# Kernel tuning notes

Hardware: AMD Instinct MI355X
Metric: run time of the kernel (lower is better)

Reference implementation:

```python
import jax, jax.numpy as jnp
import numpy as np

D_MODEL = 1024
NUM_HEADS = 16


def setup_inputs() -> dict:
    key = jax.random.key(0)
    ks = jax.random.split(key, 5)
    B, N, D = 2, 2048, D_MODEL
    x = jax.random.normal(ks[0], (B, N, D), dtype=jnp.float32)
    Wq = jax.random.normal(ks[1], (D, D), dtype=jnp.float32) * 0.02
    Wk = jax.random.normal(ks[2], (D, D), dtype=jnp.float32) * 0.02
    Wv = jax.random.normal(ks[3], (D, D), dtype=jnp.float32) * 0.02
    Wo = jax.random.normal(ks[4], (D, D), dtype=jnp.float32) * 0.02
    return {"x": x, "Wq": Wq, "Wk": Wk, "Wv": Wv, "Wo": Wo}


def reference(x, Wq, Wk, Wv, Wo):
    # Executed path of QuantizedHyperbolicAttention.forward: TRITON_AVAILABLE is
    # False in the source, so the module always runs _pytorch_attention
    # (standard scaled-dot-product attention), mask=None.
    B, N, D = x.shape
    H = NUM_HEADS
    hd = D // H
    # nn.Linear(bias=False): y = x @ W.T
    q = (x @ Wq.T).reshape(B, N, H, hd).transpose(0, 2, 1, 3)  # [B,H,N,hd]
    k = (x @ Wk.T).reshape(B, N, H, hd).transpose(0, 2, 1, 3)
    v = (x @ Wv.T).reshape(B, N, H, hd).transpose(0, 2, 1, 3)
    scale = hd ** -0.5
    attn = jnp.einsum("bhnd,bhmd->bhnm", q, k) * scale  # [B,H,N,N]
    attn = jax.nn.softmax(attn, axis=-1)
    out = jnp.einsum("bhnm,bhmd->bhnd", attn, v)  # [B,H,N,hd]
    out = out.transpose(0, 2, 1, 3).reshape(B, N, D)
    return out @ Wo.T
```

## Files before the change

kernel.cpp:

```cpp
#include <hip/hip_runtime.h>

using u16 = unsigned short;
using u32 = unsigned int;

typedef __bf16 bf16x8 __attribute__((ext_vector_type(8)));
typedef float  f32x4  __attribute__((ext_vector_type(4)));
typedef float  f32x8  __attribute__((ext_vector_type(8)));
typedef float  f32x16 __attribute__((ext_vector_type(16)));
typedef u16    u16x8  __attribute__((ext_vector_type(8)));
typedef u32    u32x4  __attribute__((ext_vector_type(4)));

#if __has_builtin(__builtin_amdgcn_exp2f)
#define QSCALE 0.1803368801f
__device__ __forceinline__ float fexp(float x) { return __builtin_amdgcn_exp2f(x); }
#else
#define QSCALE 0.125f
__device__ __forceinline__ float fexp(float x) { return __expf(x); }
#endif

__device__ __forceinline__ u32 f2bf(float f) {
  u32 u = __builtin_bit_cast(u32, f);
  return (u + 0x7fffu + ((u >> 16) & 1u)) >> 16;
}

__device__ __forceinline__ void gload_lds16(const u16* g, u16* lds) {
  __builtin_amdgcn_global_load_lds(
      (const __attribute__((address_space(1))) void*)g,
      (__attribute__((address_space(3))) void*)lds, 16, 0, 0);
}

__device__ __forceinline__ u32 cvtpk(float lo, float hi) {
  u32 r;
  asm("v_cvt_pk_bf16_f32 %0, %1, %2" : "=v"(r) : "v"(lo), "v"(hi));
  return r;
}

__device__ __forceinline__ float xhalf_add(float v) {
  return v + __shfl_xor(v, 32);
}

__global__ __launch_bounds__(256) void cvt_all(
    const float* __restrict__ x,  const float* __restrict__ wq,
    const float* __restrict__ wk, const float* __restrict__ wv,
    const float* __restrict__ wo, u16* __restrict__ out) {
  size_t i = ((size_t)blockIdx.x * 256 + threadIdx.x) * 16;
  const float* src;
  if (i < 4194304) {
    src = x + i;
  } else {
    size_t j = i - 4194304;
    unsigned w = (unsigned)(j >> 20);
    size_t o = j & 1048575;
    src = (w == 0) ? (wq + o) : (w == 1) ? (wk + o) : (w == 2) ? (wv + o) : (wo + o);
  }
  f32x4 a = *(const f32x4*)src;
  f32x4 b = *(const f32x4*)(src + 4);
  f32x4 c = *(const f32x4*)(src + 8);
  f32x4 d = *(const f32x4*)(src + 12);
  u32x4 r0, r1;
  r0[0] = f2bf(a[0]) | (f2bf(a[1]) << 16);
  r0[1] = f2bf(a[2]) | (f2bf(a[3]) << 16);
  r0[2] = f2bf(b[0]) | (f2bf(b[1]) << 16);
  r0[3] = f2bf(b[2]) | (f2bf(b[3]) << 16);
  r1[0] = f2bf(c[0]) | (f2bf(c[1]) << 16);
  r1[1] = f2bf(c[2]) | (f2bf(c[3]) << 16);
  r1[2] = f2bf(d[0]) | (f2bf(d[1]) << 16);
  r1[3] = f2bf(d[2]) | (f2bf(d[3]) << 16);
  *(u32x4*)(out + i) = r0;
  *(u32x4*)(out + i + 8) = r1;
}

template <bool F32OUT, int BM>
__device__ __forceinline__ void gemm_tile(const u16* __restrict__ A,
                                          const u16* __restrict__ Bm,
                                          void* __restrict__ Cv,
                                          int rowBase, int colBase, float scale) {
  __shared__ __align__(16) u16 As[BM * 64];
  __shared__ __align__(16) u16 Bs[128 * 64];

  const int t = threadIdx.x;
  const int lane = t & 63;
  const int wv = t >> 6;
  const int wr = (wv >> 1) * (BM / 2);
  const int wc = (wv & 1) * 64;
  const int l15 = lane & 15;
  const int lg = lane >> 4;

  f32x4 acc[BM / 32][4] = {};

  for (int kt = 0; kt < 1024; kt += 64) {
#pragma unroll
    for (int i = 0; i < BM / 32; ++i) {
      int s = i * 256 + t;
      int row = s >> 3;
      int k2 = (s & 7) ^ (row & 7);
      gload_lds16(A + (size_t)(rowBase + row) * 1024 + kt + k2 * 8,
                  &As[(i * 256 + wv * 64) * 8]);
    }
#pragma unroll
    for (int i = 0; i < 4; ++i) {
      int s = i * 256 + t;
      int row = s >> 3;
      int k2 = (s & 7) ^ (row & 7);
      gload_lds16(Bm + (size_t)(colBase + row) * 1024 + kt + k2 * 8,
                  &Bs[(i * 256 + wv * 64) * 8]);
    }
    __syncthreads();
#pragma unroll
    for (int kk = 0; kk < 2; ++kk) {
      bf16x8 af[BM / 32], bfr[4];
#pragma unroll
      for (int m = 0; m < BM / 32; ++m) {
        int row = wr + m * 16 + l15;
        af[m] = *(const bf16x8*)&As[row * 64 + (((kk * 4 + lg) ^ (row & 7)) * 8)];
      }
#pragma unroll
      for (int n = 0; n < 4; ++n) {
        int row = wc + n * 16 + l15;
        bfr[n] = *(const bf16x8*)&Bs[row * 64 + (((kk * 4 + lg) ^ (row & 7)) * 8)];
      }
      __builtin_amdgcn_s_setprio(1);
#pragma unroll
      for (int m = 0; m < BM / 32; ++m)
#pragma unroll
        for (int n = 0; n < 4; ++n)
          acc[m][n] = __builtin_amdgcn_mfma_f32_16x16x32_bf16(af[m], bfr[n], acc[m][n], 0, 0, 0);
      __builtin_amdgcn_s_setprio(0);
    }
    __syncthreads();
  }

#pragma unroll
  for (int m = 0; m < BM / 32; ++m) {
#pragma unroll
    for (int r = 0; r < 4; ++r) {
      int row = rowBase + wr + m * 16 + lg * 4 + r;
#pragma unroll
      for (int n = 0; n < 4; ++n) {
        int col = colBase + wc + n * 16 + l15;
        float v = acc[m][n][r] * scale;
        if (F32OUT)
          ((float*)Cv)[(size_t)row * 1024 + col] = v;
        else
          ((u16*)Cv)[(size_t)row * 1024 + col] = (u16)f2bf(v);
      }
    }
  }
}

__global__ __launch_bounds__(256) void gemm_qkv(
    const u16* __restrict__ xb,
    const u16* __restrict__ wq, const u16* __restrict__ wk, const u16* __restrict__ wv,
    u16* __restrict__ Qm, u16* __restrict__ Km, u16* __restrict__ Vm) {
  int bx = blockIdx.x;
  int mat = bx >> 8;
  int rem = bx & 255;
  int bm = rem & 31, bn = rem >> 5;
  const u16* B = (mat == 0) ? wq : (mat == 1) ? wk : wv;
  u16* C = (mat == 0) ? Qm : (mat == 1) ? Km : Vm;
  float scale = (mat == 0) ? QSCALE : 1.0f;
  gemm_tile<false, 128>(xb, B, C, bm * 128, bn * 128, scale);
}

__global__ __launch_bounds__(256) void gemm_out(
    const u16* __restrict__ ao, const u16* __restrict__ wo, float* __restrict__ C) {
  int bm = blockIdx.x & 63, bn = blockIdx.x >> 6;
  gemm_tile<true, 64>(ao, wo, C, bm * 64, bn * 128, 1.0f);
}

__global__ __launch_bounds__(512, 2) void attn_fwd(
    const u16* __restrict__ Q, const u16* __restrict__ K,
    const u16* __restrict__ V, u16* __restrict__ AO) {
  __shared__ __align__(16) u16 Ks[2][2][64 * 64];
  __shared__ __align__(16) u16 Vt3[2][3][64 * 64];

  const int t = threadIdx.x;
  const int lane = t & 63;
  const int wvi = t >> 6;
  const int wg = wvi & 3;
  const int grp = wvi >> 2;
  const int tg = t & 255;
  const int l31 = lane & 31;
  const int hi = lane >> 5;

  const int qb = blockIdx.x;
  const int pr = blockIdx.y;
  const size_t hb = (size_t)(pr >> 4) * 2048 * 1024 + (size_t)(pr & 15) * 64;
  const u16* Qh = Q + hb;
  const u16* Kh = K + hb;
  const u16* Vh = V + hb;
  u16* AOh = AO + hb;

  const int q0w = qb * 128 + wg * 32;
  const int kvb = grp * 1024;

  bf16x8 qf[4];
#pragma unroll
  for (int kk = 0; kk < 4; ++kk)
    qf[kk] = *(const bf16x8*)&Qh[(size_t)(q0w + l31) * 1024 + kk * 16 + hi * 8];

  f32x16 ot[2] = {};
  f32x16 sc[2];
  f32x8  Lacc = {};
  bf16x8 pa0[4], pa1[4];

  const int kxor = l31 & 7;
  const int kd0 = (l31 & 7) ^ (l31 >> 3);
  const int kv0 = (tg >> 3) * 2, d0 = (tg & 7) * 8;
  const int vg = (kv0 >> 4) * 2 + ((kv0 >> 2) & 1);
  const int vj = (kv0 & 3) + ((kv0 >> 3) & 1) * 4;

  auto VLOAD = [&](int tile, u16x8& a, u16x8& b) {
    a = *(const u16x8*)&Vh[(size_t)(kvb + tile * 64 + kv0) * 1024 + d0];
    b = *(const u16x8*)&Vh[(size_t)(kvb + tile * 64 + kv0 + 1) * 1024 + d0];
  };
  auto KSTAGE = [&](int tile, int buf) {
#pragma unroll
    for (int i = 0; i < 2; ++i) {
      int s = i * 256 + tg;
      int krow = s >> 3;
      int k2 = (s & 7) ^ (krow & 7);
      gload_lds16(&Kh[(size_t)(kvb + tile * 64 + krow) * 1024 + k2 * 8],
                  &Ks[grp][buf][(i * 256 + wg * 64) * 8]);
    }
  };
  auto VPACK = [&](u16x8 a, u16x8 b, u16* dst) {
#pragma unroll
    for (int e = 0; e < 8; ++e) {
      int d = d0 + e;
      int key = ((d & 7) ^ (d >> 3)) & 7;
      int idx = d * 64 + ((vg ^ key) * 8) + vj;
      *(u32*)&dst[idx] = (u32)a[e] | ((u32)b[e] << 16);
    }
  };
  auto QKT = [&](const u16* ks) {
    sc[0] = f32x16{};
    sc[1] = f32x16{};
    __builtin_amdgcn_s_setprio(1);
#pragma unroll
    for (int kk = 0; kk < 4; ++kk) {
      bf16x8 kf0 = *(const bf16x8*)&ks[l31 * 64 + (((kk * 2 + hi) ^ kxor) * 8)];
      bf16x8 kf1 = *(const bf16x8*)&ks[(32 + l31) * 64 + (((kk * 2 + hi) ^ kxor) * 8)];
      sc[0] = __builtin_amdgcn_mfma_f32_32x32x16_bf16(kf0, qf[kk], sc[0], 0, 0, 0);
      sc[1] = __builtin_amdgcn_mfma_f32_32x32x16_bf16(kf1, qf[kk], sc[1], 0, 0, 0);
    }
    __builtin_amdgcn_s_setprio(0);
  };
  auto PV = [&](const u16* vt, const bf16x8* pa) {
    __builtin_amdgcn_s_setprio(1);
#pragma unroll
    for (int kk = 0; kk < 4; ++kk) {
      bf16x8 vf0 = *(const bf16x8*)&vt[l31 * 64 + (((kk * 2 + hi) ^ kd0) * 8)];
      bf16x8 vf1 = *(const bf16x8*)&vt[(32 + l31) * 64 + (((kk * 2 + hi) ^ (kd0 ^ 4)) * 8)];
      ot[0] = __builtin_amdgcn_mfma_f32_32x32x16_bf16(vf0, pa[kk], ot[0], 0, 0, 0);
      ot[1] = __builtin_amdgcn_mfma_f32_32x32x16_bf16(vf1, pa[kk], ot[1], 0, 0, 0);
    }
    __builtin_amdgcn_s_setprio(0);
  };
  auto EXPPACK = [&](bf16x8* pa) {
#pragma unroll
    for (int fi = 0; fi < 2; ++fi)
#pragma unroll
      for (int r = 0; r < 16; ++r)
        sc[fi][r] = fexp(sc[fi][r]);
    {
      f32x8 lo0 = __builtin_shufflevector(sc[0], sc[0], 0,1,2,3,4,5,6,7);
      f32x8 hi0 = __builtin_shufflevector(sc[0], sc[0], 8,9,10,11,12,13,14,15);
      f32x8 lo1 = __builtin_shufflevector(sc[1], sc[1], 0,1,2,3,4,5,6,7);
      f32x8 hi1 = __builtin_shufflevector(sc[1], sc[1], 8,9,10,11,12,13,14,15);
      Lacc += (lo0 + hi0) + (lo1 + hi1);
    }
#pragma unroll
    for (int fi = 0; fi < 2; ++fi) {
      u32x4 w0 = {cvtpk(sc[fi][0],  sc[fi][1]),  cvtpk(sc[fi][2],  sc[fi][3]),
                  cvtpk(sc[fi][4],  sc[fi][5]),  cvtpk(sc[fi][6],  sc[fi][7])};
      u32x4 w1 = {cvtpk(sc[fi][8],  sc[fi][9]),  cvtpk(sc[fi][10], sc[fi][11]),
                  cvtpk(sc[fi][12], sc[fi][13]), cvtpk(sc[fi][14], sc[fi][15])};
      pa[2 * fi]     = __builtin_bit_cast(bf16x8, w0);
      pa[2 * fi + 1] = __builtin_bit_cast(bf16x8, w1);
    }
  };

  int vm1 = 2, v0 = 0, vp1 = 1;
  auto ROT = [&]() { int tmp = vm1; vm1 = v0; v0 = vp1; vp1 = tmp; };

  {
    u16x8 a, b;
    VLOAD(0, a, b);
    __builtin_amdgcn_sched_barrier(0);
    KSTAGE(0, 0);
    KSTAGE(1, 1);
    VPACK(a, b, &Vt3[grp][0][0]);
    asm volatile("s_waitcnt vmcnt(2)" ::: "memory");
    asm volatile("s_waitcnt lgkmcnt(0)" ::: "memory");
    __builtin_amdgcn_sched_barrier(0);
    __builtin_amdgcn_s_barrier();
    QKT(&Ks[grp][0][0]);
    asm volatile("s_waitcnt lgkmcnt(0)" ::: "memory");
    __builtin_amdgcn_sched_barrier(0);
    __builtin_amdgcn_s_barrier();
  }

  for (int tp = 0; tp < 7; ++tp) {
#pragma unroll
    for (int sub = 0; sub < 2; ++sub) {
      const int tt = 2 * tp + sub;
      u16x8 a, b;
      VLOAD(tt + 1, a, b);
      __builtin_amdgcn_sched_barrier(0);
      KSTAGE(tt + 2, sub);
      if (tt >= 1) PV(&Vt3[grp][vm1][0], sub ? pa0 : pa1);
      EXPPACK(sub ? pa1 : pa0);
      asm volatile("s_waitcnt vmcnt(4)" ::: "memory");
      QKT(&Ks[grp][sub ^ 1][0]);
      VPACK(a, b, &Vt3[grp][vp1][0]);
      asm volatile("s_waitcnt lgkmcnt(0)" ::: "memory");
      __builtin_amdgcn_sched_barrier(0);
      __builtin_amdgcn_s_barrier();
      ROT();
    }
  }

  {
    u16x8 a, b;
    VLOAD(15, a, b);
    __builtin_amdgcn_sched_barrier(0);
    PV(&Vt3[grp][vm1][0], pa1);
    EXPPACK(pa0);
    asm volatile("s_waitcnt vmcnt(2)" ::: "memory");
    QKT(&Ks[grp][1][0]);
    VPACK(a, b, &Vt3[grp][vp1][0]);
    asm volatile("s_waitcnt lgkmcnt(0)" ::: "memory");
    __builtin_amdgcn_sched_barrier(0);
    __builtin_amdgcn_s_barrier();
    ROT();
  }
  PV(&Vt3[grp][vm1][0], pa0);
  EXPPACK(pa1);
  ROT();
  PV(&Vt3[grp][vm1][0], pa1);

  float lp = (((Lacc[0] + Lacc[1]) + (Lacc[2] + Lacc[3])) +
              ((Lacc[4] + Lacc[5]) + (Lacc[6] + Lacc[7])));

  __syncthreads();
  float* Osh = (float*)&Ks[0][0][0];
  float* Lsh = (float*)&Vt3[0][0][0];
  const int pair = wg;
  const int obase = (((pair * 2 + hi) * 32) + l31) * 32;
  if (grp == 1) {
    *(f32x16*)&Osh[obase]      = ot[0];
    *(f32x16*)&Osh[obase + 16] = ot[1];
    Lsh[pair * 64 + lane] = lp;
  }
  __syncthreads();
  if (grp == 0) {
    ot[0] += *(const f32x16*)&Osh[obase];
    ot[1] += *(const f32x16*)&Osh[obase + 16];
    lp += Lsh[pair * 64 + lane];
    float L = xhalf_add(lp);
    float inv = 1.f / L;
    const size_t qrow = (size_t)(q0w + l31) * 1024;
#pragma unroll
    for (int dn = 0; dn < 2; ++dn)
#pragma unroll
      for (int j = 0; j < 8; ++j) {
        int r = 2 * j;
        int d = 2 * (j & 1) + 8 * (j >> 1) + 4 * hi + 32 * dn;
        u32 w = cvtpk(ot[dn][r] * inv, ot[dn][r + 1] * inv);
        *(u32*)&AOh[qrow + d] = w;
      }
  }
}

extern "C" void kernel_launch(void* const* d_in, const int* in_sizes, int n_in,
                              void* d_out, int out_size, void* d_ws, size_t ws_size,
                              hipStream_t stream) {
  const float* x  = (const float*)d_in[0];
  const float* wq = (const float*)d_in[1];
  const float* wk = (const float*)d_in[2];
  const float* wv = (const float*)d_in[3];
  const float* wo = (const float*)d_in[4];

  u16* ws = (u16*)d_ws;
  u16* xb  = ws;
  u16* wqb = ws + 4194304;
  u16* wkb = ws + 5242880;
  u16* wvb = ws + 6291456;
  u16* wob = ws + 7340032;
  u16* Qm  = ws + 8388608;
  u16* Km  = ws + 12582912;
  u16* Vm  = ws + 16777216;
  u16* AOm = ws + 20971520;

  cvt_all<<<2048, 256, 0, stream>>>(x, wq, wk, wv, wo, ws);
  gemm_qkv<<<768, 256, 0, stream>>>(xb, wqb, wkb, wvb, Qm, Km, Vm);
  attn_fwd<<<dim3(16, 32), 512, 0, stream>>>(Qm, Km, Vm, AOm);
  gemm_out<<<512, 256, 0, stream>>>(AOm, wob, (float*)d_out);
}
```

Baseline: 106.6 us.

## Drop split-KV wave groups in attention; each block scans full sequence

```diff
diff --git a/kernel.cpp b/kernel.cpp
--- a/kernel.cpp
+++ b/kernel.cpp
@@ -168,18 +168,15 @@
   gemm_tile<true, 64>(ao, wo, C, bm * 64, bn * 128, 1.0f);
 }
 
-__global__ __launch_bounds__(512, 2) void attn_fwd(
+__global__ __launch_bounds__(256, 4) void attn_fwd(
     const u16* __restrict__ Q, const u16* __restrict__ K,
     const u16* __restrict__ V, u16* __restrict__ AO) {
-  __shared__ __align__(16) u16 Ks[2][2][64 * 64];
-  __shared__ __align__(16) u16 Vt3[2][3][64 * 64];
+  __shared__ __align__(16) u16 Ks[2][64 * 64];
+  __shared__ __align__(16) u16 Vt3[3][64 * 64];
 
   const int t = threadIdx.x;
   const int lane = t & 63;
-  const int wvi = t >> 6;
-  const int wg = wvi & 3;
-  const int grp = wvi >> 2;
-  const int tg = t & 255;
+  const int wg = t >> 6;
   const int l31 = lane & 31;
   const int hi = lane >> 5;
 
@@ -192,7 +189,6 @@
   u16* AOh = AO + hb;
 
   const int q0w = qb * 128 + wg * 32;
-  const int kvb = grp * 1024;
 
   bf16x8 qf[4];
 #pragma unroll
@@ -206,22 +202,22 @@
 
   const int kxor = l31 & 7;
   const int kd0 = (l31 & 7) ^ (l31 >> 3);
-  const int kv0 = (tg >> 3) * 2, d0 = (tg & 7) * 8;
+  const int kv0 = (t >> 3) * 2, d0 = (t & 7) * 8;
   const int vg = (kv0 >> 4) * 2 + ((kv0 >> 2) & 1);
   const int vj = (kv0 & 3) + ((kv0 >> 3) & 1) * 4;
 
   auto VLOAD = [&](int tile, u16x8& a, u16x8& b) {
-    a = *(const u16x8*)&Vh[(size_t)(kvb + tile * 64 + kv0) * 1024 + d0];
-    b = *(const u16x8*)&Vh[(size_t)(kvb + tile * 64 + kv0 + 1) * 1024 + d0];
+    a = *(const u16x8*)&Vh[(size_t)(tile * 64 + kv0) * 1024 + d0];
+    b = *(const u16x8*)&Vh[(size_t)(tile * 64 + kv0 + 1) * 1024 + d0];
   };
   auto KSTAGE = [&](int tile, int buf) {
 #pragma unroll
     for (int i = 0; i < 2; ++i) {
-      int s = i * 256 + tg;
+      int s = i * 256 + t;
       int krow = s >> 3;
       int k2 = (s & 7) ^ (krow & 7);
-      gload_lds16(&Kh[(size_t)(kvb + tile * 64 + krow) * 1024 + k2 * 8],
-                  &Ks[grp][buf][(i * 256 + wg * 64) * 8]);
+      gload_lds16(&Kh[(size_t)(tile * 64 + krow) * 1024 + k2 * 8],
+                  &Ks[buf][(i * 256 + wg * 64) * 8]);
     }
   };
   auto VPACK = [&](u16x8 a, u16x8 b, u16* dst) {
@@ -290,18 +286,18 @@
     __builtin_amdgcn_sched_barrier(0);
     KSTAGE(0, 0);
     KSTAGE(1, 1);
-    VPACK(a, b, &Vt3[grp][0][0]);
+    VPACK(a, b, &Vt3[0][0]);
     asm volatile("s_waitcnt vmcnt(2)" ::: "memory");
     asm volatile("s_waitcnt lgkmcnt(0)" ::: "memory");
     __builtin_amdgcn_sched_barrier(0);
     __builtin_amdgcn_s_barrier();
-    QKT(&Ks[grp][0][0]);
+    QKT(&Ks[0][0]);
     asm volatile("s_waitcnt lgkmcnt(0)" ::: "memory");
     __builtin_amdgcn_sched_barrier(0);
     __builtin_amdgcn_s_barrier();
   }
 
-  for (int tp = 0; tp < 7; ++tp) {
+  for (int tp = 0; tp < 15; ++tp) {
 #pragma unroll
     for (int sub = 0; sub < 2; ++sub) {
       const int tt = 2 * tp + sub;
@@ -309,11 +305,11 @@
       VLOAD(tt + 1, a, b);
       __builtin_amdgcn_sched_barrier(0);
       KSTAGE(tt + 2, sub);
-      if (tt >= 1) PV(&Vt3[grp][vm1][0], sub ? pa0 : pa1);
+      if (tt >= 1) PV(&Vt3[vm1][0], sub ? pa0 : pa1);
       EXPPACK(sub ? pa1 : pa0);
       asm volatile("s_waitcnt vmcnt(4)" ::: "memory");
-      QKT(&Ks[grp][sub ^ 1][0]);
-      VPACK(a, b, &Vt3[grp][vp1][0]);
+      QKT(&Ks[sub ^ 1][0]);
+      VPACK(a, b, &Vt3[vp1][0]);
       asm volatile("s_waitcnt lgkmcnt(0)" ::: "memory");
       __builtin_amdgcn_sched_barrier(0);
       __builtin_amdgcn_s_barrier();
@@ -323,54 +319,37 @@
 
   {
     u16x8 a, b;
-    VLOAD(15, a, b);
-    __builtin_amdgcn_sched_barrier(0);
-    PV(&Vt3[grp][vm1][0], pa1);
+    VLOAD(31, a, b);
+    __builtin_amdgcn_sched_barrier(0);
+    PV(&Vt3[vm1][0], pa1);
     EXPPACK(pa0);
     asm volatile("s_waitcnt vmcnt(2)" ::: "memory");
-    QKT(&Ks[grp][1][0]);
-    VPACK(a, b, &Vt3[grp][vp1][0]);
+    QKT(&Ks[1][0]);
+    VPACK(a, b, &Vt3[vp1][0]);
     asm volatile("s_waitcnt lgkmcnt(0)" ::: "memory");
     __builtin_amdgcn_sched_barrier(0);
     __builtin_amdgcn_s_barrier();
     ROT();
   }
-  PV(&Vt3[grp][vm1][0], pa0);
+  PV(&Vt3[vm1][0], pa0);
   EXPPACK(pa1);
   ROT();
-  PV(&Vt3[grp][vm1][0], pa1);
+  PV(&Vt3[vm1][0], pa1);
 
   float lp = (((Lacc[0] + Lacc[1]) + (Lacc[2] + Lacc[3])) +
               ((Lacc[4] + Lacc[5]) + (Lacc[6] + Lacc[7])));
-
-  __syncthreads();
-  float* Osh = (float*)&Ks[0][0][0];
-  float* Lsh = (float*)&Vt3[0][0][0];
-  const int pair = wg;
-  const int obase = (((pair * 2 + hi) * 32) + l31) * 32;
-  if (grp == 1) {
-    *(f32x16*)&Osh[obase]      = ot[0];
-    *(f32x16*)&Osh[obase + 16] = ot[1];
-    Lsh[pair * 64 + lane] = lp;
-  }
-  __syncthreads();
-  if (grp == 0) {
-    ot[0] += *(const f32x16*)&Osh[obase];
-    ot[1] += *(const f32x16*)&Osh[obase + 16];
-    lp += Lsh[pair * 64 + lane];
-    float L = xhalf_add(lp);
-    float inv = 1.f / L;
-    const size_t qrow = (size_t)(q0w + l31) * 1024;
-#pragma unroll
-    for (int dn = 0; dn < 2; ++dn)
-#pragma unroll
-      for (int j = 0; j < 8; ++j) {
-        int r = 2 * j;
-        int d = 2 * (j & 1) + 8 * (j >> 1) + 4 * hi + 32 * dn;
-        u32 w = cvtpk(ot[dn][r] * inv, ot[dn][r + 1] * inv);
-        *(u32*)&AOh[qrow + d] = w;
-      }
-  }
+  float L = xhalf_add(lp);
+  float inv = 1.f / L;
+  const size_t qrow = (size_t)(q0w + l31) * 1024;
+#pragma unroll
+  for (int dn = 0; dn < 2; ++dn)
+#pragma unroll
+    for (int j = 0; j < 8; ++j) {
+      int r = 2 * j;
+      int d = 2 * (j & 1) + 8 * (j >> 1) + 4 * hi + 32 * dn;
+      u32 w = cvtpk(ot[dn][r] * inv, ot[dn][r + 1] * inv);
+      *(u32*)&AOh[qrow + d] = w;
+    }
 }
 
 extern "C" void kernel_launch(void* const* d_in, const int* in_sizes, int n_in,
@@ -395,6 +374,6 @@
 
   cvt_all<<<2048, 256, 0, stream>>>(x, wq, wk, wv, wo, ws);
   gemm_qkv<<<768, 256, 0, stream>>>(xb, wqb, wkb, wvb, Qm, Km, Vm);
-  attn_fwd<<<dim3(16, 32), 512, 0, stream>>>(Qm, Km, Vm, AOm);
+  attn_fwd<<<dim3(16, 32), 256, 0, stream>>>(Qm, Km, Vm, AOm);
   gemm_out<<<512, 256, 0, stream>>>(AOm, wob, (float*)d_out);
 }
```

New measurement: 230.1 us. +115.8%, slower.
